# Optimization experiments

Hardware: AMD Instinct MI355X
Metric: run time of the kernel (lower is better)

## Reference

```python
import jax, jax.numpy as jnp
import numpy as np

B, D, U = 8192, 1024, 1024


def setup_inputs() -> dict:
    key = jax.random.key(0)
    ks = jax.random.split(key, 11)
    scale = 0.05  # keras 'random_normal' initializer default stddev
    inp = {
        "inputs": jax.random.normal(ks[0], (B, D), jnp.float32),
        "h_tm1": jax.random.normal(ks[1], (B, U), jnp.float32),
        "c_tm1": jax.random.normal(ks[2], (B, U), jnp.float32),
        "W_i": jax.random.normal(ks[3], (D, U), jnp.float32) * scale,
        "U_i": jax.random.normal(ks[4], (U, U), jnp.float32) * scale,
        "b_i": jnp.zeros((U,), jnp.float32),
        "W_f": jax.random.normal(ks[5], (D, U), jnp.float32) * scale,
        "U_f": jax.random.normal(ks[6], (U, U), jnp.float32) * scale,
        "b_f": jnp.zeros((U,), jnp.float32),
        "W_c": jax.random.normal(ks[7], (D, U), jnp.float32) * scale,
        "U_c": jax.random.normal(ks[8], (U, U), jnp.float32) * scale,
        "b_c": jnp.zeros((U,), jnp.float32),
        "W_o": jax.random.normal(ks[9], (D, U), jnp.float32) * scale,
        "U_o": jax.random.normal(ks[10], (U, U), jnp.float32) * scale,
        "b_o": jnp.zeros((U,), jnp.float32),
    }
    return inp


def reference(inputs, h_tm1, c_tm1, W_i, U_i, b_i, W_f, U_f, b_f, W_c, U_c, b_c, W_o, U_o, b_o):
    # Concatenate the 4 gate projections into single GEMMs (same math, fused form)
    Wx = jnp.concatenate([W_i, W_f, W_c, W_o], axis=1)  # [D, 4U]
    Uh = jnp.concatenate([U_i, U_f, U_c, U_o], axis=1)  # [U, 4U]
    b = jnp.concatenate([b_i, b_f, b_c, b_o], axis=0)   # [4U]
    z = inputs @ Wx + h_tm1 @ Uh + b                     # [B, 4U]
    u = W_i.shape[1]
    zi, zf, zc, zo = z[:, :u], z[:, u:2 * u], z[:, 2 * u:3 * u], z[:, 3 * u:]
    i = jax.nn.sigmoid(zi)
    f = jax.nn.sigmoid(zf)
    c_ = jnp.tanh(zc)
    c = f * c_tm1 + i * c_
    o = jax.nn.sigmoid(zo)
    h = o * jnp.tanh(c)
    return (h, c)
```

## Files before the change

kernel.cpp:

```cpp
#include <hip/hip_runtime.h>
#include <hip/hip_bf16.h>
#include <cstdint>


using f32x4  = __attribute__((ext_vector_type(4))) float;
using short8 = __attribute__((ext_vector_type(8))) short;

__device__ __forceinline__ unsigned short f2bf(float f) {
  union { float f; unsigned int u; } v; v.f = f;
  unsigned int r = v.u + 0x7fffu + ((v.u >> 16) & 1u);
  return (unsigned short)(r >> 16);
}
__device__ __forceinline__ float sigmoidf_fast(float x) { return 1.f / (1.f + __expf(-x)); }
__device__ __forceinline__ float tanhf_fast(float x)    { return 1.f - 2.f / (__expf(2.f * x) + 1.f); }

__global__ void conv_a_kernel(const float* __restrict__ X, const float* __restrict__ H,
                              unsigned short* __restrict__ Ap) {
  __shared__ float tile[256][36];
  int kt = blockIdx.x;
  int bm = blockIdx.y;
  const float* src = (kt < 32) ? X : H;
  int kbase = (kt & 31) * 32;
  int t = threadIdx.x;
#pragma unroll
  for (int i = 0; i < 8; ++i) {
    int flat = i * 256 + t;
    int row = flat >> 3;
    int kq  = (flat & 7) * 4;
    float4 v = *(const float4*)(src + (long)(bm * 256 + row) * 1024 + kbase + kq);
    tile[row][kq]     = v.x; tile[row][kq + 1] = v.y;
    tile[row][kq + 2] = v.z; tile[row][kq + 3] = v.w;
  }
  __syncthreads();
  long obase = (long)(bm * 64 + kt) * 8192;
#pragma unroll
  for (int i = 0; i < 4; ++i) {
    int p = i * 256 + t;
    int f = p >> 6, l = p & 63;
    int row = f * 16 + (l & 15);
    int kc  = (l >> 4) * 8;
    float4 v0 = *(const float4*)&tile[row][kc];
    float4 v1 = *(const float4*)&tile[row][kc + 4];
    unsigned short ov[8];
    ov[0] = f2bf(v0.x); ov[1] = f2bf(v0.y); ov[2] = f2bf(v0.z); ov[3] = f2bf(v0.w);
    ov[4] = f2bf(v1.x); ov[5] = f2bf(v1.y); ov[6] = f2bf(v1.z); ov[7] = f2bf(v1.w);
    *(uint4*)(Ap + obase + (long)p * 8) = *(uint4*)ov;
  }
}

__global__ void conv_b_kernel(const float* W_i, const float* U_i,
                              const float* W_f, const float* U_f,
                              const float* W_c, const float* U_c,
                              const float* W_o, const float* U_o,
                              unsigned short* __restrict__ Bt) {
  __shared__ float tile[64][65];
  int z = blockIdx.z;
  const float* src;
  switch (z) {
    case 0: src = W_i; break; case 1: src = U_i; break;
    case 2: src = W_f; break; case 3: src = U_f; break;
    case 4: src = W_c; break; case 5: src = U_c; break;
    case 6: src = W_o; break; default: src = U_o; break;
  }
  int g = z >> 1, s = z & 1;
  int k0 = blockIdx.x * 64;
  int u0 = blockIdx.y * 64;
  int t = threadIdx.x;
  int c = t & 63, r0 = t >> 6;
#pragma unroll
  for (int i = 0; i < 16; ++i) {
    int r = i * 4 + r0;
    tile[r][c] = src[(long)(k0 + r) * 1024 + u0 + c];
  }
  __syncthreads();
  int ul = t >> 2;
  int ks = (t & 3) * 16;
  unsigned short outv[16];
#pragma unroll
  for (int j = 0; j < 16; ++j) outv[j] = f2bf(tile[ks + j][ul]);
  long n   = 4L * u0 + (ul >> 4) * 64 + g * 16 + (ul & 15);
  long col = (long)s * 1024 + k0 + ks;
  uint4* dst = (uint4*)(Bt + n * 2048 + col);
  dst[0] = *(uint4*)(outv);
  dst[1] = *(uint4*)(outv + 8);
}

__global__ __launch_bounds__(512, 2) void lstm_gemm_kernel(
    const unsigned short* __restrict__ Ap,
    const unsigned short* __restrict__ Btbf,
    const float* __restrict__ b_i, const float* __restrict__ b_f,
    const float* __restrict__ b_c, const float* __restrict__ b_o,
    const float* __restrict__ c_tm1,
    float* __restrict__ outH, float* __restrict__ outC) {
  __shared__ unsigned short smem[3 * 8192];

  int bid = blockIdx.x;
  int swz = (bid & 7) * 64 + (bid >> 3);
  int bm = swz >> 4;
  int bn = swz & 15;

  int t = threadIdx.x;
  int lane = t & 63;
  int w = t >> 6;
  int wm = w >> 1;
  int wn = w & 1;
  int rl = lane & 15;
  int kg = lane >> 4;

#define BOFFE(NI) (((wn * 128 + (NI) * 16 + rl) * 32) + \
    ((kg ^ (((wn * 128 + (NI) * 16 + rl) >> 1) & 3)) << 3))
  const int offB0 = BOFFE(0), offB1 = BOFFE(1), offB2 = BOFFE(2), offB3 = BOFFE(3);
  const int offB4 = BOFFE(4), offB5 = BOFFE(5), offB6 = BOFFE(6), offB7 = BOFFE(7);
#undef BOFFE

  const unsigned short* gA = Ap + ((long)bm * 64 * 16 + wm * 4) * 512 + lane * 8;

  int srow = t >> 2;
  int cbe  = ((t & 3) ^ ((srow >> 1) & 3)) << 3;
  const unsigned short* bS0 = Btbf + (long)(bn * 256 + srow) * 2048 + cbe;
  const unsigned short* bS1 = bS0 + 128L * 2048;
  const int dB = t * 8;

#define GLL(SRC, DELM)                                                                     \
  __builtin_amdgcn_global_load_lds((const __attribute__((address_space(1))) void*)(SRC),   \
      (__attribute__((address_space(3))) void*)(&smem[DELM]), 16, 0, 0)
#define GLLB(SB, KOFF)                                                         \
  do {                                                                         \
    GLL(bS0 + (KOFF), (SB) * 8192 + dB);                                       \
    GLL(bS1 + (KOFF), (SB) * 8192 + 4096 + dB);                                \
  } while (0)
#define VMC(N) asm volatile("s_waitcnt vmcnt(" #N ")" ::: "memory")

  f32x4 acc[4][8];
#pragma unroll
  for (int mi = 0; mi < 4; ++mi)
#pragma unroll
    for (int ni = 0; ni < 8; ++ni) acc[mi][ni] = (f32x4){0.f, 0.f, 0.f, 0.f};

  short8 pa0, pa1, pa2, pa3;
  short8 qa0, qa1, qa2, qa3;
  short8 bb0, bb1, bb2, bb3, bb4, bb5, bb6, bb7;

#define LOADA(S, KOFF)                                                         \
  do {                                                                         \
    S##a0 = *(const short8*)(gA + (KOFF));                                     \
    S##a1 = *(const short8*)(gA + (KOFF) + 512);                               \
    S##a2 = *(const short8*)(gA + (KOFF) + 1024);                              \
    S##a3 = *(const short8*)(gA + (KOFF) + 1536);                              \
  } while (0)

#define MF8(AF, MI)                                                                      \
  acc[MI][0] = __builtin_amdgcn_mfma_f32_16x16x32_bf16(AF, bb0, acc[MI][0], 0, 0, 0);    \
  acc[MI][1] = __builtin_amdgcn_mfma_f32_16x16x32_bf16(AF, bb1, acc[MI][1], 0, 0, 0);    \
  acc[MI][2] = __builtin_amdgcn_mfma_f32_16x16x32_bf16(AF, bb2, acc[MI][2], 0, 0, 0);    \
  acc[MI][3] = __builtin_amdgcn_mfma_f32_16x16x32_bf16(AF, bb3, acc[MI][3], 0, 0, 0);    \
  acc[MI][4] = __builtin_amdgcn_mfma_f32_16x16x32_bf16(AF, bb4, acc[MI][4], 0, 0, 0);    \
  acc[MI][5] = __builtin_amdgcn_mfma_f32_16x16x32_bf16(AF, bb5, acc[MI][5], 0, 0, 0);    \
  acc[MI][6] = __builtin_amdgcn_mfma_f32_16x16x32_bf16(AF, bb6, acc[MI][6], 0, 0, 0);    \
  acc[MI][7] = __builtin_amdgcn_mfma_f32_16x16x32_bf16(AF, bb7, acc[MI][7], 0, 0, 0);

#define WINDOW(RB, SB, KOA, KOB, C, N, DOA, DOST, VMN, DOBAR)                  \
  {                                                                            \
    if (DOA) LOADA(N, KOA);                                                    \
    const unsigned short* S_ = smem + (RB) * 8192;                             \
    bb0 = *(const short8*)(S_ + offB0);                                        \
    bb1 = *(const short8*)(S_ + offB1);                                        \
    bb2 = *(const short8*)(S_ + offB2);                                        \
    bb3 = *(const short8*)(S_ + offB3);                                        \
    bb4 = *(const short8*)(S_ + offB4);                                        \
    bb5 = *(const short8*)(S_ + offB5);                                        \
    bb6 = *(const short8*)(S_ + offB6);                                        \
    bb7 = *(const short8*)(S_ + offB7);                                        \
    if (DOST) GLLB(SB, KOB);                                                   \
    __builtin_amdgcn_s_setprio(1);                                             \
    MF8(C##a0, 0) MF8(C##a1, 1) MF8(C##a2, 2) MF8(C##a3, 3)                    \
    __builtin_amdgcn_s_setprio(0);                                             \
    if ((VMN) == 6) VMC(6);                                                    \
    if ((VMN) == 4) VMC(4);                                                    \
    if ((VMN) == 0) VMC(0);                                                    \
    if (DOBAR) __builtin_amdgcn_s_barrier();                                   \
  }

  GLLB(0, 0);
  GLLB(1, 32);
  LOADA(p, 0);
  VMC(6);
  __builtin_amdgcn_s_barrier();
  bS0 += 64; bS1 += 64;

  for (int g = 0; g < 10; ++g) {
    WINDOW(0, 2, 8192,  0,   p, q, 1, 1, 6, 1);
    WINDOW(1, 0, 16384, 32,  q, p, 1, 1, 6, 1);
    WINDOW(2, 1, 24576, 64,  p, q, 1, 1, 6, 1);
    WINDOW(0, 2, 32768, 96,  q, p, 1, 1, 6, 1);
    WINDOW(1, 0, 40960, 128, p, q, 1, 1, 6, 1);
    WINDOW(2, 1, 49152, 160, q, p, 1, 1, 6, 1);
    gA += 49152; bS0 += 192; bS1 += 192;
  }
  WINDOW(0, 2, 8192,  0,  p, q, 1, 1, 6, 1);
  WINDOW(1, 0, 16384, 32, q, p, 1, 1, 6, 1);
  WINDOW(2, 0, 24576, 0,  p, q, 1, 0, 4, 1);
  WINDOW(0, 0, 0,     0,  q, p, 0, 0, -1, 0);
#undef WINDOW
#undef MF8
#undef LOADA
#undef VMC
#undef GLLB
#undef GLL

  int mbase = bm * 256 + wm * 64;
  int nbase = bn * 256 + wn * 128;
  int ub = nbase >> 2;
  int u0 = ub + rl;
  int u1 = ub + 16 + rl;
  float bi0 = b_i[u0], bf0 = b_f[u0], bc0 = b_c[u0], bo0 = b_o[u0];
  float bi1 = b_i[u1], bf1 = b_f[u1], bc1 = b_c[u1], bo1 = b_o[u1];
  int rquad = kg << 2;
#pragma unroll
  for (int mi = 0; mi < 4; ++mi) {
#pragma unroll
    for (int j = 0; j < 4; ++j) {
      int brow = mbase + mi * 16 + rquad + j;
      {
        float zi = acc[mi][0][j] + bi0;
        float zf = acc[mi][1][j] + bf0;
        float zc = acc[mi][2][j] + bc0;
        float zo = acc[mi][3][j] + bo0;
        float ig = sigmoidf_fast(zi);
        float fg = sigmoidf_fast(zf);
        float cg = tanhf_fast(zc);
        float og = sigmoidf_fast(zo);
        float cp = c_tm1[(long)brow * 1024 + u0];
        float cn = fg * cp + ig * cg;
        float hn = og * tanhf_fast(cn);
        outH[(long)brow * 1024 + u0] = hn;
        outC[(long)brow * 1024 + u0] = cn;
      }
      {
        float zi = acc[mi][4][j] + bi1;
        float zf = acc[mi][5][j] + bf1;
        float zc = acc[mi][6][j] + bc1;
        float zo = acc[mi][7][j] + bo1;
        float ig = sigmoidf_fast(zi);
        float fg = sigmoidf_fast(zf);
        float cg = tanhf_fast(zc);
        float og = sigmoidf_fast(zo);
        float cp = c_tm1[(long)brow * 1024 + u1];
        float cn = fg * cp + ig * cg;
        float hn = og * tanhf_fast(cn);
        outH[(long)brow * 1024 + u1] = hn;
        outC[(long)brow * 1024 + u1] = cn;
      }
    }
  }
}

extern "C" void kernel_launch(void* const* d_in, const int* in_sizes, int n_in,
                              void* d_out, int out_size, void* d_ws, size_t ws_size,
                              hipStream_t stream) {
  (void)in_sizes; (void)n_in; (void)out_size; (void)ws_size;
  const float* X   = (const float*)d_in[0];
  const float* Hst = (const float*)d_in[1];
  const float* Cst = (const float*)d_in[2];
  const float* W_i = (const float*)d_in[3];
  const float* U_i = (const float*)d_in[4];
  const float* b_i = (const float*)d_in[5];
  const float* W_f = (const float*)d_in[6];
  const float* U_f = (const float*)d_in[7];
  const float* b_f = (const float*)d_in[8];
  const float* W_c = (const float*)d_in[9];
  const float* U_c = (const float*)d_in[10];
  const float* b_c = (const float*)d_in[11];
  const float* W_o = (const float*)d_in[12];
  const float* U_o = (const float*)d_in[13];
  const float* b_o = (const float*)d_in[14];

  unsigned short* Ap   = (unsigned short*)d_ws;
  unsigned short* Btbf = (unsigned short*)((char*)d_ws + 33554432);

  float* outH = (float*)d_out;
  float* outC = outH + 8192L * 1024;

  conv_a_kernel<<<dim3(64, 32), 256, 0, stream>>>(X, Hst, Ap);
  conv_b_kernel<<<dim3(16, 16, 8), 256, 0, stream>>>(W_i, U_i, W_f, U_f, W_c, U_c, W_o, U_o, Btbf);
  lstm_gemm_kernel<<<512, 512, 0, stream>>>(Ap, Btbf, b_i, b_f, b_c, b_o, Cst, outH, outC);
}
```

Before: 161.7 us.

## Pre-pack B into MFMA fragment layout and load both operands directly from global

The weight conversion kernel now writes B in the same per-fragment packed layout as A, so each lane can read its MFMA operand with one contiguous 16-byte load. The GEMM drops LDS staging, global_load_lds, waitcnts and barriers and instead double-buffers A and B fragments in registers. This removes LDS traffic and synchronisation. In exchange, each wave now fetches its B tiles from global memory or L2 on its own, with no sharing through LDS across the two wave rows, and register pressure rises.

```diff
diff --git a/kernel.cpp b/kernel.cpp
--- a/kernel.cpp
+++ b/kernel.cpp
@@ -52,7 +52,7 @@
                               const float* W_f, const float* U_f,
                               const float* W_c, const float* U_c,
                               const float* W_o, const float* U_o,
-                              unsigned short* __restrict__ Bt) {
+                              unsigned short* __restrict__ Bp) {
   __shared__ float tile[64][65];
   int z = blockIdx.z;
   const float* src;
@@ -78,22 +78,26 @@
   unsigned short outv[16];
 #pragma unroll
   for (int j = 0; j < 16; ++j) outv[j] = f2bf(tile[ks + j][ul]);
-  long n   = 4L * u0 + (ul >> 4) * 64 + g * 16 + (ul & 15);
+  int u = u0 + ul;
+  long n   = 4L * (u >> 4) * 16 + (long)(u >> 4) * 0 + ((long)(u >> 4) * 64) + g * 16 + (u & 15);
+  n = ((long)(u >> 4)) * 64 + g * 16 + (u & 15);
   long col = (long)s * 1024 + k0 + ks;
-  uint4* dst = (uint4*)(Bt + n * 2048 + col);
-  dst[0] = *(uint4*)(outv);
-  dst[1] = *(uint4*)(outv + 8);
+  int kt = (int)(col >> 5);
+  int bnb = (int)(n >> 8);
+  int f   = (int)((n >> 4) & 15);
+  int l0  = (int)((n & 15) + (((col >> 3) & 3) << 4));
+  long base = ((long)(bnb * 64 + kt) * 16 + f) * 512;
+  *(uint4*)(Bp + base + (long)l0 * 8)        = *(uint4*)(outv);
+  *(uint4*)(Bp + base + (long)(l0 + 16) * 8) = *(uint4*)(outv + 8);
 }
 
 __global__ __launch_bounds__(512, 2) void lstm_gemm_kernel(
     const unsigned short* __restrict__ Ap,
-    const unsigned short* __restrict__ Btbf,
+    const unsigned short* __restrict__ Bp,
     const float* __restrict__ b_i, const float* __restrict__ b_f,
     const float* __restrict__ b_c, const float* __restrict__ b_o,
     const float* __restrict__ c_tm1,
     float* __restrict__ outH, float* __restrict__ outC) {
-  __shared__ unsigned short smem[3 * 8192];
-
   int bid = blockIdx.x;
   int swz = (bid & 7) * 64 + (bid >> 3);
   int bm = swz >> 4;
@@ -107,106 +111,63 @@
   int rl = lane & 15;
   int kg = lane >> 4;
 
-#define BOFFE(NI) (((wn * 128 + (NI) * 16 + rl) * 32) + \
-    ((kg ^ (((wn * 128 + (NI) * 16 + rl) >> 1) & 3)) << 3))
-  const int offB0 = BOFFE(0), offB1 = BOFFE(1), offB2 = BOFFE(2), offB3 = BOFFE(3);
-  const int offB4 = BOFFE(4), offB5 = BOFFE(5), offB6 = BOFFE(6), offB7 = BOFFE(7);
-#undef BOFFE
-
   const unsigned short* gA = Ap + ((long)bm * 64 * 16 + wm * 4) * 512 + lane * 8;
-
-  int srow = t >> 2;
-  int cbe  = ((t & 3) ^ ((srow >> 1) & 3)) << 3;
-  const unsigned short* bS0 = Btbf + (long)(bn * 256 + srow) * 2048 + cbe;
-  const unsigned short* bS1 = bS0 + 128L * 2048;
-  const int dB = t * 8;
-
-#define GLL(SRC, DELM)                                                                     \
-  __builtin_amdgcn_global_load_lds((const __attribute__((address_space(1))) void*)(SRC),   \
-      (__attribute__((address_space(3))) void*)(&smem[DELM]), 16, 0, 0)
-#define GLLB(SB, KOFF)                                                         \
+  const unsigned short* gB = Bp + ((long)bn * 64 * 16 + wn * 8) * 512 + lane * 8;
+
+  f32x4 acc[4][8];
+#pragma unroll
+  for (int mi = 0; mi < 4; ++mi)
+#pragma unroll
+    for (int ni = 0; ni < 8; ++ni) acc[mi][ni] = (f32x4){0.f, 0.f, 0.f, 0.f};
+
+  short8 pa0, pa1, pa2, pa3, pb0, pb1, pb2, pb3, pb4, pb5, pb6, pb7;
+  short8 qa0, qa1, qa2, qa3, qb0, qb1, qb2, qb3, qb4, qb5, qb6, qb7;
+
+#define LOADSET(S, KO)                                                         \
   do {                                                                         \
-    GLL(bS0 + (KOFF), (SB) * 8192 + dB);                                       \
-    GLL(bS1 + (KOFF), (SB) * 8192 + 4096 + dB);                                \
+    S##a0 = *(const short8*)(gA + (KO));                                       \
+    S##a1 = *(const short8*)(gA + (KO) + 512);                                 \
+    S##a2 = *(const short8*)(gA + (KO) + 1024);                                \
+    S##a3 = *(const short8*)(gA + (KO) + 1536);                                \
+    S##b0 = *(const short8*)(gB + (KO));                                       \
+    S##b1 = *(const short8*)(gB + (KO) + 512);                                 \
+    S##b2 = *(const short8*)(gB + (KO) + 1024);                                \
+    S##b3 = *(const short8*)(gB + (KO) + 1536);                                \
+    S##b4 = *(const short8*)(gB + (KO) + 2048);                                \
+    S##b5 = *(const short8*)(gB + (KO) + 2560);                                \
+    S##b6 = *(const short8*)(gB + (KO) + 3072);                                \
+    S##b7 = *(const short8*)(gB + (KO) + 3584);                                \
   } while (0)
-#define VMC(N) asm volatile("s_waitcnt vmcnt(" #N ")" ::: "memory")
-
-  f32x4 acc[4][8];
-#pragma unroll
-  for (int mi = 0; mi < 4; ++mi)
-#pragma unroll
-    for (int ni = 0; ni < 8; ++ni) acc[mi][ni] = (f32x4){0.f, 0.f, 0.f, 0.f};
-
-  short8 pa0, pa1, pa2, pa3;
-  short8 qa0, qa1, qa2, qa3;
-  short8 bb0, bb1, bb2, bb3, bb4, bb5, bb6, bb7;
-
-#define LOADA(S, KOFF)                                                         \
-  do {                                                                         \
-    S##a0 = *(const short8*)(gA + (KOFF));                                     \
-    S##a1 = *(const short8*)(gA + (KOFF) + 512);                               \
-    S##a2 = *(const short8*)(gA + (KOFF) + 1024);                              \
-    S##a3 = *(const short8*)(gA + (KOFF) + 1536);                              \
-  } while (0)
-
-#define MF8(AF, MI)                                                                      \
-  acc[MI][0] = __builtin_amdgcn_mfma_f32_16x16x32_bf16(AF, bb0, acc[MI][0], 0, 0, 0);    \
-  acc[MI][1] = __builtin_amdgcn_mfma_f32_16x16x32_bf16(AF, bb1, acc[MI][1], 0, 0, 0);    \
-  acc[MI][2] = __builtin_amdgcn_mfma_f32_16x16x32_bf16(AF, bb2, acc[MI][2], 0, 0, 0);    \
-  acc[MI][3] = __builtin_amdgcn_mfma_f32_16x16x32_bf16(AF, bb3, acc[MI][3], 0, 0, 0);    \
-  acc[MI][4] = __builtin_amdgcn_mfma_f32_16x16x32_bf16(AF, bb4, acc[MI][4], 0, 0, 0);    \
-  acc[MI][5] = __builtin_amdgcn_mfma_f32_16x16x32_bf16(AF, bb5, acc[MI][5], 0, 0, 0);    \
-  acc[MI][6] = __builtin_amdgcn_mfma_f32_16x16x32_bf16(AF, bb6, acc[MI][6], 0, 0, 0);    \
-  acc[MI][7] = __builtin_amdgcn_mfma_f32_16x16x32_bf16(AF, bb7, acc[MI][7], 0, 0, 0);
-
-#define WINDOW(RB, SB, KOA, KOB, C, N, DOA, DOST, VMN, DOBAR)                  \
-  {                                                                            \
-    if (DOA) LOADA(N, KOA);                                                    \
-    const unsigned short* S_ = smem + (RB) * 8192;                             \
-    bb0 = *(const short8*)(S_ + offB0);                                        \
-    bb1 = *(const short8*)(S_ + offB1);                                        \
-    bb2 = *(const short8*)(S_ + offB2);                                        \
-    bb3 = *(const short8*)(S_ + offB3);                                        \
-    bb4 = *(const short8*)(S_ + offB4);                                        \
-    bb5 = *(const short8*)(S_ + offB5);                                        \
-    bb6 = *(const short8*)(S_ + offB6);                                        \
-    bb7 = *(const short8*)(S_ + offB7);                                        \
-    if (DOST) GLLB(SB, KOB);                                                   \
-    __builtin_amdgcn_s_setprio(1);                                             \
-    MF8(C##a0, 0) MF8(C##a1, 1) MF8(C##a2, 2) MF8(C##a3, 3)                    \
-    __builtin_amdgcn_s_setprio(0);                                             \
-    if ((VMN) == 6) VMC(6);                                                    \
-    if ((VMN) == 4) VMC(4);                                                    \
-    if ((VMN) == 0) VMC(0);                                                    \
-    if (DOBAR) __builtin_amdgcn_s_barrier();                                   \
-  }
-
-  GLLB(0, 0);
-  GLLB(1, 32);
-  LOADA(p, 0);
-  VMC(6);
-  __builtin_amdgcn_s_barrier();
-  bS0 += 64; bS1 += 64;
-
-  for (int g = 0; g < 10; ++g) {
-    WINDOW(0, 2, 8192,  0,   p, q, 1, 1, 6, 1);
-    WINDOW(1, 0, 16384, 32,  q, p, 1, 1, 6, 1);
-    WINDOW(2, 1, 24576, 64,  p, q, 1, 1, 6, 1);
-    WINDOW(0, 2, 32768, 96,  q, p, 1, 1, 6, 1);
-    WINDOW(1, 0, 40960, 128, p, q, 1, 1, 6, 1);
-    WINDOW(2, 1, 49152, 160, q, p, 1, 1, 6, 1);
-    gA += 49152; bS0 += 192; bS1 += 192;
-  }
-  WINDOW(0, 2, 8192,  0,  p, q, 1, 1, 6, 1);
-  WINDOW(1, 0, 16384, 32, q, p, 1, 1, 6, 1);
-  WINDOW(2, 0, 24576, 0,  p, q, 1, 0, 4, 1);
-  WINDOW(0, 0, 0,     0,  q, p, 0, 0, -1, 0);
-#undef WINDOW
+
+#define MF8(AF, MI, S)                                                                       \
+  acc[MI][0] = __builtin_amdgcn_mfma_f32_16x16x32_bf16(AF, S##b0, acc[MI][0], 0, 0, 0);      \
+  acc[MI][1] = __builtin_amdgcn_mfma_f32_16x16x32_bf16(AF, S##b1, acc[MI][1], 0, 0, 0);      \
+  acc[MI][2] = __builtin_amdgcn_mfma_f32_16x16x32_bf16(AF, S##b2, acc[MI][2], 0, 0, 0);      \
+  acc[MI][3] = __builtin_amdgcn_mfma_f32_16x16x32_bf16(AF, S##b3, acc[MI][3], 0, 0, 0);      \
+  acc[MI][4] = __builtin_amdgcn_mfma_f32_16x16x32_bf16(AF, S##b4, acc[MI][4], 0, 0, 0);      \
+  acc[MI][5] = __builtin_amdgcn_mfma_f32_16x16x32_bf16(AF, S##b5, acc[MI][5], 0, 0, 0);      \
+  acc[MI][6] = __builtin_amdgcn_mfma_f32_16x16x32_bf16(AF, S##b6, acc[MI][6], 0, 0, 0);      \
+  acc[MI][7] = __builtin_amdgcn_mfma_f32_16x16x32_bf16(AF, S##b7, acc[MI][7], 0, 0, 0);
+
+#define MFALL(S)                                                               \
+  __builtin_amdgcn_s_setprio(1);                                               \
+  MF8(S##a0, 0, S) MF8(S##a1, 1, S) MF8(S##a2, 2, S) MF8(S##a3, 3, S)          \
+  __builtin_amdgcn_s_setprio(0);
+
+  LOADSET(p, 0);
+  for (int i = 0; i < 31; ++i) {
+    LOADSET(q, 8192);
+    MFALL(p)
+    LOADSET(p, 16384);
+    MFALL(q)
+    gA += 16384; gB += 16384;
+  }
+  LOADSET(q, 8192);
+  MFALL(p)
+  MFALL(q)
+#undef MFALL
 #undef MF8
-#undef LOADA
-#undef VMC
-#undef GLLB
-#undef GLL
+#undef LOADSET
 
   int mbase = bm * 256 + wm * 64;
   int nbase = bn * 256 + wn * 128;
@@ -275,13 +236,13 @@
   const float* U_o = (const float*)d_in[13];
   const float* b_o = (const float*)d_in[14];
 
-  unsigned short* Ap   = (unsigned short*)d_ws;
-  unsigned short* Btbf = (unsigned short*)((char*)d_ws + 33554432);
+  unsigned short* Ap = (unsigned short*)d_ws;
+  unsigned short* Bp = (unsigned short*)((char*)d_ws + 33554432);
 
   float* outH = (float*)d_out;
   float* outC = outH + 8192L * 1024;
 
   conv_a_kernel<<<dim3(64, 32), 256, 0, stream>>>(X, Hst, Ap);
-  conv_b_kernel<<<dim3(16, 16, 8), 256, 0, stream>>>(W_i, U_i, W_f, U_f, W_c, U_c, W_o, U_o, Btbf);
-  lstm_gemm_kernel<<<512, 512, 0, stream>>>(Ap, Btbf, b_i, b_f, b_c, b_o, Cst, outH, outC);
-}
+  conv_b_kernel<<<dim3(16, 16, 8), 256, 0, stream>>>(W_i, U_i, W_f, U_f, W_c, U_c, W_o, U_o, Bp);
+  lstm_gemm_kernel<<<512, 512, 0, stream>>>(Ap, Bp, b_i, b_f, b_c, b_o, Cst, outH, outC);
+}
```

Measured after the change: 165.1 us. 2.1% more time.
